# Kernel tuning notes

Hardware: AMD Instinct MI355X
Metric: run time of the kernel (lower is better)

## Reference

```python
import jax, jax.numpy as jnp
import numpy as np

N, F_IN, H, C, D, NH, L, FF = 4096, 256, 2, 64, 128, 4, 2, 2048
DEG = 32


def setup_inputs() -> dict:
    key = jax.random.key(0)
    ks = jax.random.split(key, 32)
    s = 0.05
    # graph: random edges + self loops (PyG GATConv adds self loops)
    src = jax.random.randint(ks[0], (N * DEG,), 0, N)
    dst = jax.random.randint(ks[1], (N * DEG,), 0, N)
    loop = jnp.arange(N)
    edge_index = jnp.stack([jnp.concatenate([src, loop]),
                            jnp.concatenate([dst, loop])]).astype(jnp.int64)
    inp = {
        'x': jax.random.normal(ks[2], (N, F_IN), jnp.float32),
        'edge_index': edge_index,
        'enc_w1': jax.random.normal(ks[3], (F_IN, 128), jnp.float32) * s,
        'enc_b1': jnp.zeros((128,), jnp.float32),
        'enc_w2': jax.random.normal(ks[4], (128, D), jnp.float32) * s,
        'enc_b2': jnp.zeros((D,), jnp.float32),
        'gat_w': jax.random.normal(ks[5], (D, H * C), jnp.float32) * s,
        'gat_asrc': jax.random.normal(ks[6], (H, C), jnp.float32) * s,
        'gat_adst': jax.random.normal(ks[7], (H, C), jnp.float32) * s,
        'gat_bias': jnp.zeros((H * C,), jnp.float32),
        't_wq': jax.random.normal(ks[8], (L, D, D), jnp.float32) * s,
        't_bq': jnp.zeros((L, D), jnp.float32),
        't_wk': jax.random.normal(ks[9], (L, D, D), jnp.float32) * s,
        't_bk': jnp.zeros((L, D), jnp.float32),
        't_wv': jax.random.normal(ks[10], (L, D, D), jnp.float32) * s,
        't_bv': jnp.zeros((L, D), jnp.float32),
        't_wo': jax.random.normal(ks[11], (L, D, D), jnp.float32) * s,
        't_bo': jnp.zeros((L, D), jnp.float32),
        't_ln1_g': jnp.ones((L, D), jnp.float32),
        't_ln1_b': jnp.zeros((L, D), jnp.float32),
        't_ln2_g': jnp.ones((L, D), jnp.float32),
        't_ln2_b': jnp.zeros((L, D), jnp.float32),
        't_w1': jax.random.normal(ks[12], (L, D, FF), jnp.float32) * s,
        't_b1': jnp.zeros((L, FF), jnp.float32),
        't_w2': jax.random.normal(ks[13], (L, FF, D), jnp.float32) * s,
        't_b2': jnp.zeros((L, D), jnp.float32),
    }
    return inp


def _layer_norm(v, g, b):
    m = v.mean(-1, keepdims=True)
    var = v.var(-1, keepdims=True)
    return (v - m) / jnp.sqrt(var + 1e-5) * g + b


def _forward(x, edge_index, enc_w1, enc_b1, enc_w2, enc_b2,
             gat_w, gat_asrc, gat_adst, gat_bias,
             t_wq, t_bq, t_wk, t_bk, t_wv, t_bv, t_wo, t_bo,
             t_ln1_g, t_ln1_b, t_ln2_g, t_ln2_b, t_w1, t_b1, t_w2, t_b2):
    n = x.shape[0]
    # encoder MLP: Linear -> ReLU -> Linear
    h = jnp.maximum(x @ enc_w1 + enc_b1, 0.0) @ enc_w2 + enc_b2  # [N, D]
    # GATConv (concat heads), dropout inactive (eval)
    heads, ch = gat_asrc.shape
    hh = (h @ gat_w).reshape(n, heads, ch)                       # [N, H, C]
    src, dst = edge_index[0], edge_index[1]
    a_src = (hh * gat_asrc).sum(-1)                              # [N, H]
    a_dst = (hh * gat_adst).sum(-1)
    e = jax.nn.leaky_relu(a_src[src] + a_dst[dst], 0.2)          # [E, H]
    # segment softmax over destination nodes
    e_max = jax.ops.segment_max(e, dst, num_segments=n)
    e_exp = jnp.exp(e - e_max[dst])
    denom = jax.ops.segment_sum(e_exp, dst, num_segments=n)
    alpha = e_exp / denom[dst]                                   # [E, H]
    agg = jax.ops.segment_sum(alpha[:, :, None] * hh[src], dst, num_segments=n)
    y = agg.reshape(n, heads * ch) + gat_bias                    # [N, D]
    # TransformerEncoder (post-LN, relu FFN), unbatched sequence of N nodes
    d = y.shape[-1]
    dh = d // NH
    for l in range(t_wq.shape[0]):
        q = (y @ t_wq[l] + t_bq[l]).reshape(n, NH, dh)
        k = (y @ t_wk[l] + t_bk[l]).reshape(n, NH, dh)
        v = (y @ t_wv[l] + t_bv[l]).reshape(n, NH, dh)
        scores = jnp.einsum('nhd,mhd->hnm', q, k) / jnp.sqrt(jnp.float32(dh))
        p = jax.nn.softmax(scores, axis=-1)
        a = jnp.einsum('hnm,mhd->nhd', p, v).reshape(n, d)
        a = a @ t_wo[l] + t_bo[l]
        y = _layer_norm(y + a, t_ln1_g[l], t_ln1_b[l])
        f = jnp.maximum(y @ t_w1[l] + t_b1[l], 0.0) @ t_w2[l] + t_b2[l]
        y = _layer_norm(y + f, t_ln2_g[l], t_ln2_b[l])
    return y


def reference(x, edge_index, enc_w1, enc_b1, enc_w2, enc_b2,
              gat_w, gat_asrc, gat_adst, gat_bias,
              t_wq, t_bq, t_wk, t_bk, t_wv, t_bv, t_wo, t_bo,
              t_ln1_g, t_ln1_b, t_ln2_g, t_ln2_b, t_w1, t_b1, t_w2, t_b2):
    return _forward(x, edge_index, enc_w1, enc_b1, enc_w2, enc_b2,
                    gat_w, gat_asrc, gat_adst, gat_bias,
                    t_wq, t_bq, t_wk, t_bk, t_wv, t_bv, t_wo, t_bo,
                    t_ln1_g, t_ln1_b, t_ln2_g, t_ln2_b, t_w1, t_b1, t_w2, t_b2)
```

## Files before the change

### kernel.cpp

```cpp
#include <hip/hip_runtime.h>

typedef unsigned short u16;
typedef unsigned int u32;
typedef __attribute__((ext_vector_type(8))) short bh8;
typedef __attribute__((ext_vector_type(4))) float fx4;
typedef __attribute__((ext_vector_type(4))) short s4;

#define QS 0.2550437194342803f

__device__ __forceinline__ u16 f2bf(float f) {
    unsigned u = __float_as_uint(f);
    u += 0x7fffu + ((u >> 16) & 1u);
    return (u16)(u >> 16);
}

__global__ __launch_bounds__(256) void prep_kernel(
    const float* x, const float* ew1, const float* ew2, const float* gw,
    const float* wq, const float* wk, const float* wv, const float* wo,
    const float* w1, const float* w2,
    const float* bq, const float* bk, const float* bv,
    u16* xb, u16* ew1t, u16* ew2t, u16* gwt,
    u16* wqkvt, float* bqkv, u16* wot, u16* w1t, u16* w2t)
{
    __shared__ u16 tile[64 * 65];
    int bid = blockIdx.x;
    const int t = threadIdx.x;

    if (bid < 128) {
        const float4* x4 = (const float4*)x;
        s4* o4 = (s4*)xb;
        #pragma unroll
        for (int i = 0; i < 8; i++) {
            int fi = bid * 2048 + i * 256 + t;
            float4 v = x4[fi];
            s4 o = { (short)f2bf(v.x), (short)f2bf(v.y), (short)f2bf(v.z), (short)f2bf(v.w) };
            o4[fi] = o;
        }
        return;
    }
    bid -= 128;
    if (bid < 1) {
        for (int idx = t; idx < 768; idx += 256) {
            int l = idx / 384, n = idx % 384;
            float v;
            if (n < 128)      v = bq[l * 128 + n] * QS;
            else if (n < 256) v = bk[l * 128 + n - 128];
            else              v = bv[l * 128 + n - 256];
            bqkv[idx] = v;
        }
        return;
    }
    bid -= 1;

    const float* src; u16* dst; int R, C, tr, tc; float sc = 1.f;
    if (bid < 8)            { src = ew1; dst = ew1t; R = 256; C = 128; tr = bid >> 1; tc = bid & 1; }
    else if ((bid -= 8) < 4)  { src = ew2; dst = ew2t; R = 128; C = 128; tr = bid >> 1; tc = bid & 1; }
    else if ((bid -= 4) < 4)  { src = gw;  dst = gwt;  R = 128; C = 128; tr = bid >> 1; tc = bid & 1; }
    else if ((bid -= 4) < 24) {
        int l = bid / 12, r2 = bid % 12, which = r2 >> 2, i = r2 & 3;
        R = 128; C = 128; tr = i >> 1; tc = i & 1;
        if (which == 0)      { src = wq + l * 16384; dst = wqkvt + l * 49152;         sc = QS; }
        else if (which == 1) { src = wk + l * 16384; dst = wqkvt + l * 49152 + 16384; }
        else                 { src = wv + l * 16384; dst = wqkvt + l * 49152 + 32768; }
    }
    else if ((bid -= 24) < 8)   { int l = bid >> 2, i = bid & 3;  src = wo + l * 16384; dst = wot + l * 16384; R = 128; C = 128; tr = i >> 1; tc = i & 1; }
    else if ((bid -= 8) < 128)  { int l = bid >> 6, i = bid & 63; src = w1 + (size_t)l * 262144; dst = w1t + (size_t)l * 262144; R = 128;  C = 2048; tr = i & 1;  tc = i >> 1; }
    else { bid -= 128;            int l = bid >> 6, i = bid & 63; src = w2 + (size_t)l * 262144; dst = w2t + (size_t)l * 262144; R = 2048; C = 128;  tr = i >> 1; tc = i & 1; }

    const int r = t >> 2, cs = (t & 3) * 16;
    const float* sp = src + (size_t)(tr * 64 + r) * C + tc * 64 + cs;
    #pragma unroll
    for (int j = 0; j < 16; j++) tile[r * 65 + cs + j] = f2bf(sp[j] * sc);
    __syncthreads();
    u16* dp = dst + (size_t)(tc * 64 + r) * R + tr * 64 + cs;
    #pragma unroll
    for (int j = 0; j < 16; j++) dp[j] = tile[(cs + j) * 65 + r];
}

__global__ __launch_bounds__(256) void gemm_bf16(
    const u16* __restrict__ A, const u16* __restrict__ Bt,
    const float* __restrict__ bias,
    float* __restrict__ Cf, u16* __restrict__ Cb, float* __restrict__ Cpart,
    u16* __restrict__ Cvt,
    int M, int N, int K, int relu, int kchunk, int ldc)
{
    __shared__ __align__(16) u16 As[2][64][40];
    __shared__ __align__(16) u16 Bs[2][64][40];
    const int m0 = blockIdx.x * 64, n0 = blockIdx.y * 64, z = blockIdx.z;
    const int tid = threadIdx.x;
    const int lane = tid & 63, w = tid >> 6;
    const int wm = (w >> 1) * 32, wn = (w & 1) * 32;
    const int l15 = lane & 15, l4 = lane >> 4;
    const int srow = tid >> 2, skq = (tid & 3) * 8;
    const int k0 = z * kchunk;

    const u16* Ap = A + (size_t)(m0 + srow) * K + k0 + skq;
    const u16* Bp = Bt + (size_t)(n0 + srow) * K + k0 + skq;

    fx4 acc00 = {0,0,0,0}, acc01 = {0,0,0,0}, acc10 = {0,0,0,0}, acc11 = {0,0,0,0};

    *(int4*)&As[0][srow][skq] = *(const int4*)Ap;
    *(int4*)&Bs[0][srow][skq] = *(const int4*)Bp;

    const int niter = kchunk >> 5;
    for (int it = 0; it < niter; it++) {
        const int cur = it & 1;
        int4 ar, br;
        __syncthreads();
        if (it + 1 < niter) {
            ar = *(const int4*)(Ap + (it + 1) * 32);
            br = *(const int4*)(Bp + (it + 1) * 32);
        }
        bh8 a0 = *(const bh8*)&As[cur][wm + l15][l4 * 8];
        bh8 a1 = *(const bh8*)&As[cur][wm + 16 + l15][l4 * 8];
        bh8 b0 = *(const bh8*)&Bs[cur][wn + l15][l4 * 8];
        bh8 b1 = *(const bh8*)&Bs[cur][wn + 16 + l15][l4 * 8];
        acc00 = __builtin_amdgcn_mfma_f32_16x16x32_bf16(a0, b0, acc00, 0, 0, 0);
        acc01 = __builtin_amdgcn_mfma_f32_16x16x32_bf16(a0, b1, acc01, 0, 0, 0);
        acc10 = __builtin_amdgcn_mfma_f32_16x16x32_bf16(a1, b0, acc10, 0, 0, 0);
        acc11 = __builtin_amdgcn_mfma_f32_16x16x32_bf16(a1, b1, acc11, 0, 0, 0);
        if (it + 1 < niter) {
            *(int4*)&As[cur ^ 1][srow][skq] = ar;
            *(int4*)&Bs[cur ^ 1][srow][skq] = br;
        }
    }

    fx4* accs[2][2] = {{&acc00, &acc01}, {&acc10, &acc11}};
    #pragma unroll
    for (int i = 0; i < 2; i++)
        #pragma unroll
        for (int j = 0; j < 2; j++) {
            int colg = n0 + wn + j * 16 + l15;
            int rowb = m0 + wm + i * 16 + l4 * 4;
            if (Cpart) {
                float* cp = Cpart + (size_t)z * M * N;
                #pragma unroll
                for (int r = 0; r < 4; r++)
                    cp[(size_t)(rowb + r) * N + colg] = (*accs[i][j])[r];
                continue;
            }
            float bvv = bias ? bias[colg] : 0.f;
            float vals[4];
            #pragma unroll
            for (int r = 0; r < 4; r++) {
                float v = (*accs[i][j])[r] + bvv;
                vals[r] = relu ? fmaxf(v, 0.f) : v;
            }
            if (Cvt && colg >= 256) {
                s4 pk = { (short)f2bf(vals[0]), (short)f2bf(vals[1]),
                          (short)f2bf(vals[2]), (short)f2bf(vals[3]) };
                *(s4*)&Cvt[(size_t)(colg - 256) * 4096 + rowb] = pk;
            } else {
                #pragma unroll
                for (int r = 0; r < 4; r++) {
                    if (Cf) Cf[(size_t)(rowb + r) * ldc + colg] = vals[r];
                    if (Cb) Cb[(size_t)(rowb + r) * ldc + colg] = f2bf(vals[r]);
                }
            }
        }
}

__global__ __launch_bounds__(128) void gat_prep(
    const float* __restrict__ hh, const float* __restrict__ asrc,
    const float* __restrict__ adst, float* __restrict__ an_src,
    float* __restrict__ an_dst)
{
    int n = blockIdx.x, tid = threadIdx.x;
    int head = tid >> 6, c = tid & 63;
    float v = hh[n * 128 + tid];
    float ps = v * asrc[head * 64 + c];
    float pd = v * adst[head * 64 + c];
    for (int off = 32; off; off >>= 1) { ps += __shfl_down(ps, off); pd += __shfl_down(pd, off); }
    if (c == 0) { an_src[n * 2 + head] = ps; an_dst[n * 2 + head] = pd; }
}

__global__ void count_edges(const int* __restrict__ dst, int* counts, int E) {
    int i = blockIdx.x * 256 + threadIdx.x;
    if (i < E) atomicAdd(&counts[dst[i]], 1);
}

__global__ __launch_bounds__(1024) void scan_kernel(const int* __restrict__ counts,
                                                    int* row_start, int* cursor) {
    __shared__ int s[1024];
    int tid = threadIdx.x, b = tid * 4;
    int c0 = counts[b], c1 = counts[b+1], c2 = counts[b+2], c3 = counts[b+3];
    int sum = c0 + c1 + c2 + c3;
    s[tid] = sum;
    __syncthreads();
    for (int off = 1; off < 1024; off <<= 1) {
        int v = (tid >= off) ? s[tid - off] : 0;
        __syncthreads();
        s[tid] += v;
        __syncthreads();
    }
    int excl = s[tid] - sum;
    int r0 = excl, r1 = excl + c0, r2 = r1 + c1, r3 = r2 + c2;
    row_start[b] = r0; row_start[b+1] = r1; row_start[b+2] = r2; row_start[b+3] = r3;
    cursor[b] = r0; cursor[b+1] = r1; cursor[b+2] = r2; cursor[b+3] = r3;
    if (tid == 1023) row_start[4096] = s[1023];
}

__global__ void scatter_edges(const int* __restrict__ src, const int* __restrict__ dst,
                              int* cursor, int* csr_src, int E) {
    int i = blockIdx.x * 256 + threadIdx.x;
    if (i < E) { int pos = atomicAdd(&cursor[dst[i]], 1); csr_src[pos] = src[i]; }
}

__global__ __launch_bounds__(128) void gat_aggregate(
    const int* __restrict__ row_start, const int* __restrict__ csr_src,
    const float* __restrict__ an_src, const float* __restrict__ an_dst,
    const float* __restrict__ hh, const float* __restrict__ gbias,
    float* __restrict__ y32, u16* __restrict__ yb)
{
    int n = blockIdx.x, tid = threadIdx.x;
    int start = row_start[n], end = row_start[n + 1];
    float ad0 = an_dst[n * 2 + 0], ad1 = an_dst[n * 2 + 1];

    float mx0 = -1e30f, mx1 = -1e30f;
    for (int i = start + tid; i < end; i += 128) {
        int s = csr_src[i];
        float e0 = an_src[s * 2 + 0] + ad0; e0 = e0 > 0.f ? e0 : 0.2f * e0;
        float e1 = an_src[s * 2 + 1] + ad1; e1 = e1 > 0.f ? e1 : 0.2f * e1;
        mx0 = fmaxf(mx0, e0); mx1 = fmaxf(mx1, e1);
    }
    for (int off = 32; off; off >>= 1) { mx0 = fmaxf(mx0, __shfl_down(mx0, off)); mx1 = fmaxf(mx1, __shfl_down(mx1, off)); }
    __shared__ float sm[2][2];
    if ((tid & 63) == 0) { sm[tid >> 6][0] = mx0; sm[tid >> 6][1] = mx1; }
    __syncthreads();
    mx0 = fmaxf(sm[0][0], sm[1][0]); mx1 = fmaxf(sm[0][1], sm[1][1]);

    float s0 = 0.f, s1 = 0.f;
    for (int i = start + tid; i < end; i += 128) {
        int s = csr_src[i];
        float e0 = an_src[s * 2 + 0] + ad0; e0 = e0 > 0.f ? e0 : 0.2f * e0;
        float e1 = an_src[s * 2 + 1] + ad1; e1 = e1 > 0.f ? e1 : 0.2f * e1;
        s0 += __expf(e0 - mx0); s1 += __expf(e1 - mx1);
    }
    for (int off = 32; off; off >>= 1) { s0 += __shfl_down(s0, off); s1 += __shfl_down(s1, off); }
    __shared__ float ss[2][2];
    if ((tid & 63) == 0) { ss[tid >> 6][0] = s0; ss[tid >> 6][1] = s1; }
    __syncthreads();
    s0 = ss[0][0] + ss[1][0]; s1 = ss[0][1] + ss[1][1];

    int head = tid >> 6, c = tid & 63;
    float mx = head ? mx1 : mx0, dn = head ? s1 : s0, ad = head ? ad1 : ad0;
    float agg = 0.f;
    for (int i = start; i < end; i++) {
        int s = csr_src[i];
        float e = an_src[s * 2 + head] + ad; e = e > 0.f ? e : 0.2f * e;
        agg += (__expf(e - mx) / dn) * hh[(size_t)s * 128 + head * 64 + c];
    }
    float v = agg + gbias[tid];
    y32[(size_t)n * 128 + tid] = v;
    yb[(size_t)n * 128 + tid] = f2bf(v);
}

__global__ __launch_bounds__(256) void flash_attn_part(
    const u16* __restrict__ q, const u16* __restrict__ k,
    const u16* __restrict__ vt, float* __restrict__ po,
    float* __restrict__ pm, float* __restrict__ pl)
{
    __shared__ __align__(16) u16 Kb[2][64][40];
    __shared__ __align__(16) u16 Vb[2][32][72];
    __shared__ __align__(16) u16 Ps[4][16][72];
    const int q0 = blockIdx.x * 64, h = blockIdx.y, ch = blockIdx.z;
    const int tid = threadIdx.x;
    const int w = tid >> 6, lane = tid & 63, l15 = lane & 15, l4 = lane >> 4;

    bh8 qf = *(const bh8*)&q[(size_t)(q0 + w * 16 + l15) * 256 + h * 32 + l4 * 8];

    const int skey = tid >> 2, sds = (tid & 3) * 8;
    const int svd = tid >> 3, svk = (tid & 7) * 8;
    const u16* kgp = &k[(size_t)(ch * 512 + skey) * 256 + h * 32 + sds];
    const u16* vgp = &vt[(size_t)(h * 32 + svd) * 4096 + ch * 512 + svk];

    fx4 o0 = {0,0,0,0}, o1 = {0,0,0,0};
    float M = -1e30f, L = 0.f;

    *(int4*)&Kb[0][skey][sds] = *(const int4*)kgp;
    *(int4*)&Vb[0][svd][svk] = *(const int4*)vgp;

    for (int ti = 0; ti < 8; ti++) {
        const int cur = ti & 1;
        int4 kr, vr;
        __syncthreads();
        if (ti < 7) {
            kr = *(const int4*)(kgp + (size_t)(ti + 1) * 64 * 256);
            vr = *(const int4*)(vgp + (ti + 1) * 64);
        }

        fx4 s[4];
        #pragma unroll
        for (int sub = 0; sub < 4; sub++) {
            bh8 kf = *(const bh8*)&Kb[cur][sub * 16 + l15][l4 * 8];
            fx4 z = {0,0,0,0};
            s[sub] = __builtin_amdgcn_mfma_f32_16x16x32_bf16(kf, qf, z, 0, 0, 0);
        }
        float m = fmaxf(fmaxf(s[0][0], s[0][1]), fmaxf(s[0][2], s[0][3]));
        #pragma unroll
        for (int sub = 1; sub < 4; sub++)
            m = fmaxf(m, fmaxf(fmaxf(s[sub][0], s[sub][1]), fmaxf(s[sub][2], s[sub][3])));
        m = fmaxf(m, __shfl_xor(m, 16));
        m = fmaxf(m, __shfl_xor(m, 32));
        float Mn = fmaxf(M, m);
        float f = __builtin_amdgcn_exp2f(M - Mn);
        M = Mn;
        o0 *= f; o1 *= f; L *= f;

        float lsum = 0.f;
        #pragma unroll
        for (int sub = 0; sub < 4; sub++)
            #pragma unroll
            for (int r = 0; r < 4; r++) {
                float pv = __builtin_amdgcn_exp2f(s[sub][r] - M);
                s[sub][r] = pv;
                lsum += pv;
            }
        lsum += __shfl_xor(lsum, 16);
        lsum += __shfl_xor(lsum, 32);
        L += lsum;

        #pragma unroll
        for (int sub = 0; sub < 4; sub++) {
            u32 w0 = (u32)f2bf(s[sub][0]) | ((u32)f2bf(s[sub][1]) << 16);
            u32 w1 = (u32)f2bf(s[sub][2]) | ((u32)f2bf(s[sub][3]) << 16);
            *(u32*)&Ps[w][l15][sub * 16 + l4 * 4]     = w0;
            *(u32*)&Ps[w][l15][sub * 16 + l4 * 4 + 2] = w1;
        }

        #pragma unroll
        for (int kc = 0; kc < 2; kc++) {
            bh8 bf  = *(const bh8*)&Ps[w][l15][kc * 32 + l4 * 8];
            bh8 af0 = *(const bh8*)&Vb[cur][l15][kc * 32 + l4 * 8];
            bh8 af1 = *(const bh8*)&Vb[cur][16 + l15][kc * 32 + l4 * 8];
            o0 = __builtin_amdgcn_mfma_f32_16x16x32_bf16(af0, bf, o0, 0, 0, 0);
            o1 = __builtin_amdgcn_mfma_f32_16x16x32_bf16(af1, bf, o1, 0, 0, 0);
        }

        if (ti < 7) {
            *(int4*)&Kb[cur ^ 1][skey][sds] = kr;
            *(int4*)&Vb[cur ^ 1][svd][svk] = vr;
        }
    }
    const int base = (blockIdx.x * 4 + h) * 8 + ch;
    const int qrow = w * 16 + l15;
    *(fx4*)&po[(size_t)(base * 64 + qrow) * 32 + l4 * 4]      = o0;
    *(fx4*)&po[(size_t)(base * 64 + qrow) * 32 + 16 + l4 * 4] = o1;
    if (l4 == 0) { pm[base * 64 + qrow] = M; pl[base * 64 + qrow] = L; }
}

__global__ __launch_bounds__(256) void attn_combine(
    const float* __restrict__ po, const float* __restrict__ pm,
    const float* __restrict__ pl, u16* __restrict__ out)
{
    int qb = blockIdx.x, h = blockIdx.y;
    int col = threadIdx.x & 31, r0 = threadIdx.x >> 5;
    int rb = (qb * 4 + h) * 8;
    for (int j = 0; j < 8; j++) {
        int row = r0 * 8 + j;
        float m = -1e30f;
        for (int c = 0; c < 8; c++) m = fmaxf(m, pm[(rb + c) * 64 + row]);
        float l = 0.f, o = 0.f;
        for (int c = 0; c < 8; c++) {
            float wgt = __builtin_amdgcn_exp2f(pm[(rb + c) * 64 + row] - m);
            l += wgt * pl[(rb + c) * 64 + row];
            o += wgt * po[(size_t)((rb + c) * 64 + row) * 32 + col];
        }
        out[(size_t)(qb * 64 + row) * 128 + h * 32 + col] = f2bf(o / l);
    }
}

__global__ __launch_bounds__(128) void add_ln(
    const float* __restrict__ y, const float* __restrict__ delta,
    const float* __restrict__ g, const float* __restrict__ b,
    float* __restrict__ out32, u16* __restrict__ outb)
{
    int n = blockIdx.x, tid = threadIdx.x;
    float v = y[(size_t)n * 128 + tid] + delta[(size_t)n * 128 + tid];
    float sacc = v;
    for (int off = 32; off; off >>= 1) sacc += __shfl_down(sacc, off);
    __shared__ float sm[2], sv[2];
    if ((tid & 63) == 0) sm[tid >> 6] = sacc;
    __syncthreads();
    float mean = (sm[0] + sm[1]) * (1.f / 128.f);
    float d = v - mean;
    float qacc = d * d;
    for (int off = 32; off; off >>= 1) qacc += __shfl_down(qacc, off);
    if ((tid & 63) == 0) sv[tid >> 6] = qacc;
    __syncthreads();
    float var = (sv[0] + sv[1]) * (1.f / 128.f);
    float o = d * rsqrtf(var + 1e-5f) * g[tid] + b[tid];
    out32[(size_t)n * 128 + tid] = o;
    outb[(size_t)n * 128 + tid] = f2bf(o);
}

__global__ __launch_bounds__(128) void add_ln8(
    const float* __restrict__ y, const float* __restrict__ part,
    const float* __restrict__ bias,
    const float* __restrict__ g, const float* __restrict__ b,
    float* __restrict__ out32, u16* __restrict__ outb)
{
    int n = blockIdx.x, tid = threadIdx.x;
    float v = y[(size_t)n * 128 + tid] + bias[tid];
    for (int z = 0; z < 8; z++) v += part[(size_t)z * 524288 + n * 128 + tid];
    float sacc = v;
    for (int off = 32; off; off >>= 1) sacc += __shfl_down(sacc, off);
    __shared__ float sm[2], sv[2];
    if ((tid & 63) == 0) sm[tid >> 6] = sacc;
    __syncthreads();
    float mean = (sm[0] + sm[1]) * (1.f / 128.f);
    float d = v - mean;
    float qacc = d * d;
    for (int off = 32; off; off >>= 1) qacc += __shfl_down(qacc, off);
    if ((tid & 63) == 0) sv[tid >> 6] = qacc;
    __syncthreads();
    float var = (sv[0] + sv[1]) * (1.f / 128.f);
    float o = d * rsqrtf(var + 1e-5f) * g[tid] + b[tid];
    out32[(size_t)n * 128 + tid] = o;
    outb[(size_t)n * 128 + tid] = f2bf(o);
}

extern "C" void kernel_launch(void* const* d_in, const int* in_sizes, int n_in,
                              void* d_out, int out_size, void* d_ws, size_t ws_size,
                              hipStream_t stream)
{
    const float* x     = (const float*)d_in[0];
    const int*   ei    = (const int*)  d_in[1];
    const float* ew1   = (const float*)d_in[2];
    const float* eb1   = (const float*)d_in[3];
    const float* ew2   = (const float*)d_in[4];
    const float* eb2   = (const float*)d_in[5];
    const float* gw    = (const float*)d_in[6];
    const float* gasrc = (const float*)d_in[7];
    const float* gadst = (const float*)d_in[8];
    const float* gbias = (const float*)d_in[9];
    const float* wq    = (const float*)d_in[10];
    const float* bq    = (const float*)d_in[11];
    const float* wk    = (const float*)d_in[12];
    const float* bk    = (const float*)d_in[13];
    const float* wv    = (const float*)d_in[14];
    const float* bv    = (const float*)d_in[15];
    const float* wo    = (const float*)d_in[16];
    const float* bo    = (const float*)d_in[17];
    const float* ln1g  = (const float*)d_in[18];
    const float* ln1b  = (const float*)d_in[19];
    const float* ln2g  = (const float*)d_in[20];
    const float* ln2b  = (const float*)d_in[21];
    const float* w1    = (const float*)d_in[22];
    const float* b1    = (const float*)d_in[23];
    const float* w2    = (const float*)d_in[24];
    const float* b2    = (const float*)d_in[25];

    const int E = in_sizes[1] / 2;
    const int* esrc = ei;
    const int* edst = ei + E;

    char* p = (char*)d_ws;
    auto alloc = [&](size_t bytes) -> void* {
        void* r = (void*)p;
        p += (bytes + 255) & ~(size_t)255;
        return r;
    };
    u16* xb    = (u16*)alloc(4096 * 256 * 2);
    u16* ew1t  = (u16*)alloc(128 * 256 * 2);
    u16* ew2t  = (u16*)alloc(128 * 128 * 2);
    u16* gwt   = (u16*)alloc(128 * 128 * 2);
    u16* wqkvt = (u16*)alloc(2 * 384 * 128 * 2);
    float* bqkv = (float*)alloc(2 * 384 * 4);
    u16* wot   = (u16*)alloc(2 * 128 * 128 * 2);
    u16* w1t   = (u16*)alloc(2 * 2048 * 128 * 2);
    u16* w2t   = (u16*)alloc(2 * 128 * 2048 * 2);
    u16* h1b   = (u16*)alloc(4096 * 128 * 2);
    u16* hb    = (u16*)alloc(4096 * 128 * 2);
    float* hh  = (float*)alloc(4096 * 128 * 4);
    float* ansrc = (float*)alloc(4096 * 2 * 4);
    float* andst = (float*)alloc(4096 * 2 * 4);
    int* counts    = (int*)alloc(4096 * 4);
    int* row_start = (int*)alloc(4097 * 4);
    int* cursor    = (int*)alloc(4096 * 4);
    int* csr_src   = (int*)alloc((size_t)E * 4);
    float* y32 = (float*)alloc(4096 * 128 * 4);
    u16* yb    = (u16*)alloc(4096 * 128 * 2);
    u16* qkvb  = (u16*)alloc((size_t)4096 * 256 * 2);
    u16* vtb   = (u16*)alloc(4096 * 128 * 2);
    u16* attnb = (u16*)alloc(4096 * 128 * 2);
    float* po  = (float*)alloc((size_t)64 * 4 * 8 * 64 * 32 * 4);
    float* pm  = (float*)alloc(64 * 4 * 8 * 64 * 4);
    float* pl  = (float*)alloc(64 * 4 * 8 * 64 * 4);
    float* proj32 = (float*)alloc(4096 * 128 * 4);
    u16* ff1b  = (u16*)alloc((size_t)4096 * 2048 * 2);
    float* ff2part = (float*)alloc((size_t)8 * 4096 * 128 * 4);

    prep_kernel<<<433, 256, 0, stream>>>(x, ew1, ew2, gw, wq, wk, wv, wo, w1, w2,
                                         bq, bk, bv,
                                         xb, ew1t, ew2t, gwt, wqkvt, bqkv, wot, w1t, w2t);

    gemm_bf16<<<dim3(64, 2), 256, 0, stream>>>(xb, ew1t, eb1, nullptr, h1b, nullptr, nullptr, 4096, 128, 256, 1, 256, 128);
    gemm_bf16<<<dim3(64, 2), 256, 0, stream>>>(h1b, ew2t, eb2, nullptr, hb, nullptr, nullptr, 4096, 128, 128, 0, 128, 128);

    gemm_bf16<<<dim3(64, 2), 256, 0, stream>>>(hb, gwt, nullptr, hh, nullptr, nullptr, nullptr, 4096, 128, 128, 0, 128, 128);
    gat_prep<<<4096, 128, 0, stream>>>(hh, gasrc, gadst, ansrc, andst);
    hipMemsetAsync(counts, 0, 4096 * sizeof(int), stream);
    count_edges<<<(E + 255) / 256, 256, 0, stream>>>(edst, counts, E);
    scan_kernel<<<1, 1024, 0, stream>>>(counts, row_start, cursor);
    scatter_edges<<<(E + 255) / 256, 256, 0, stream>>>(esrc, edst, cursor, csr_src, E);
    gat_aggregate<<<4096, 128, 0, stream>>>(row_start, csr_src, ansrc, andst, hh, gbias, y32, yb);

    for (int l = 0; l < 2; l++) {
        gemm_bf16<<<dim3(64, 6), 256, 0, stream>>>(yb, wqkvt + l * 49152, bqkv + l * 384, nullptr, qkvb, nullptr, vtb, 4096, 384, 128, 0, 128, 256);
        flash_attn_part<<<dim3(64, 4, 8), 256, 0, stream>>>(qkvb, qkvb + 128, vtb, po, pm, pl);
        attn_combine<<<dim3(64, 4), 256, 0, stream>>>(po, pm, pl, attnb);
        gemm_bf16<<<dim3(64, 2), 256, 0, stream>>>(attnb, wot + l * 16384, bo + l * 128, proj32, nullptr, nullptr, nullptr, 4096, 128, 128, 0, 128, 128);
        add_ln<<<4096, 128, 0, stream>>>(y32, proj32, ln1g + l * 128, ln1b + l * 128, y32, yb);
        gemm_bf16<<<dim3(64, 32), 256, 0, stream>>>(yb, w1t + (size_t)l * 262144, b1 + l * 2048, nullptr, ff1b, nullptr, nullptr, 4096, 2048, 128, 1, 128, 2048);
        gemm_bf16<<<dim3(64, 2, 8), 256, 0, stream>>>(ff1b, w2t + (size_t)l * 262144, nullptr, nullptr, nullptr, ff2part, nullptr, 4096, 128, 2048, 0, 256, 128);
        float* outp = (l == 1) ? (float*)d_out : y32;
        add_ln8<<<4096, 128, 0, stream>>>(y32, ff2part, b2 + l * 128, ln2g + l * 128, ln2b + l * 128, outp, yb);
    }
}
```

Baseline: 216.3 us.

## Template GEMM tile sizes per call and widen GAT aggregation blocks

Turns the fixed 64x64 bf16 MFMA GEMM into a template over block tile sizes. Each call now gets its own tile: 128x128 for the FFN GEMMs for more register reuse, and 32x64 for the small 128-wide GEMMs to launch more blocks. The GAT aggregation goes from 128 to 256 threads, splitting the edge loop across two groups and adding a shared-memory reduction at the end. Flash-attention LDS padding also changes from 72 to 68. Larger tiles raise register pressure and cut the block count for the FFN GEMMs, and the 68 padding may alter LDS bank conflicts.

```diff
diff --git a/kernel.cpp b/kernel.cpp
--- a/kernel.cpp
+++ b/kernel.cpp
@@ -77,73 +77,80 @@
     for (int j = 0; j < 16; j++) dp[j] = tile[(cs + j) * 65 + r];
 }
 
-__global__ __launch_bounds__(256) void gemm_bf16(
+template<int BM, int BN>
+__global__ __launch_bounds__(256) void gemm_t(
     const u16* __restrict__ A, const u16* __restrict__ Bt,
     const float* __restrict__ bias,
     float* __restrict__ Cf, u16* __restrict__ Cb, float* __restrict__ Cpart,
     u16* __restrict__ Cvt,
     int M, int N, int K, int relu, int kchunk, int ldc)
 {
-    __shared__ __align__(16) u16 As[2][64][40];
-    __shared__ __align__(16) u16 Bs[2][64][40];
-    const int m0 = blockIdx.x * 64, n0 = blockIdx.y * 64, z = blockIdx.z;
+    constexpr int NM = BM / 32, NN = BN / 32;
+    constexpr int ASL = BM * 4, BSL = BN * 4;
+    constexpr int ANI = (ASL + 255) / 256, BNI = (BSL + 255) / 256;
+    __shared__ __align__(16) u16 As[2][BM][40];
+    __shared__ __align__(16) u16 Bs[2][BN][40];
+    const int m0 = blockIdx.x * BM, n0 = blockIdx.y * BN, z = blockIdx.z;
     const int tid = threadIdx.x;
     const int lane = tid & 63, w = tid >> 6;
-    const int wm = (w >> 1) * 32, wn = (w & 1) * 32;
+    const int wm = (w >> 1) * (BM / 2), wn = (w & 1) * (BN / 2);
     const int l15 = lane & 15, l4 = lane >> 4;
-    const int srow = tid >> 2, skq = (tid & 3) * 8;
     const int k0 = z * kchunk;
 
-    const u16* Ap = A + (size_t)(m0 + srow) * K + k0 + skq;
-    const u16* Bp = Bt + (size_t)(n0 + srow) * K + k0 + skq;
-
-    fx4 acc00 = {0,0,0,0}, acc01 = {0,0,0,0}, acc10 = {0,0,0,0}, acc11 = {0,0,0,0};
-
-    *(int4*)&As[0][srow][skq] = *(const int4*)Ap;
-    *(int4*)&Bs[0][srow][skq] = *(const int4*)Bp;
+    fx4 acc[NM][NN] = {};
+
+    #pragma unroll
+    for (int i = 0; i < ANI; i++) { int s = tid + i * 256; if (s < ASL) { int r = s >> 2, c = (s & 3) * 8; *(int4*)&As[0][r][c] = *(const int4*)&A[(size_t)(m0 + r) * K + k0 + c]; } }
+    #pragma unroll
+    for (int i = 0; i < BNI; i++) { int s = tid + i * 256; if (s < BSL) { int r = s >> 2, c = (s & 3) * 8; *(int4*)&Bs[0][r][c] = *(const int4*)&Bt[(size_t)(n0 + r) * K + k0 + c]; } }
 
     const int niter = kchunk >> 5;
     for (int it = 0; it < niter; it++) {
         const int cur = it & 1;
-        int4 ar, br;
+        int4 ar[ANI], br[BNI];
         __syncthreads();
         if (it + 1 < niter) {
-            ar = *(const int4*)(Ap + (it + 1) * 32);
-            br = *(const int4*)(Bp + (it + 1) * 32);
-        }
-        bh8 a0 = *(const bh8*)&As[cur][wm + l15][l4 * 8];
-        bh8 a1 = *(const bh8*)&As[cur][wm + 16 + l15][l4 * 8];
-        bh8 b0 = *(const bh8*)&Bs[cur][wn + l15][l4 * 8];
-        bh8 b1 = *(const bh8*)&Bs[cur][wn + 16 + l15][l4 * 8];
-        acc00 = __builtin_amdgcn_mfma_f32_16x16x32_bf16(a0, b0, acc00, 0, 0, 0);
-        acc01 = __builtin_amdgcn_mfma_f32_16x16x32_bf16(a0, b1, acc01, 0, 0, 0);
-        acc10 = __builtin_amdgcn_mfma_f32_16x16x32_bf16(a1, b0, acc10, 0, 0, 0);
-        acc11 = __builtin_amdgcn_mfma_f32_16x16x32_bf16(a1, b1, acc11, 0, 0, 0);
+            #pragma unroll
+            for (int i = 0; i < ANI; i++) { int s = tid + i * 256; if (s < ASL) { int r = s >> 2, c = (s & 3) * 8; ar[i] = *(const int4*)&A[(size_t)(m0 + r) * K + k0 + (it + 1) * 32 + c]; } }
+            #pragma unroll
+            for (int i = 0; i < BNI; i++) { int s = tid + i * 256; if (s < BSL) { int r = s >> 2, c = (s & 3) * 8; br[i] = *(const int4*)&Bt[(size_t)(n0 + r) * K + k0 + (it + 1) * 32 + c]; } }
+        }
+        bh8 af[NM], bf[NN];
+        #pragma unroll
+        for (int mi = 0; mi < NM; mi++) af[mi] = *(const bh8*)&As[cur][wm + mi * 16 + l15][l4 * 8];
+        #pragma unroll
+        for (int nj = 0; nj < NN; nj++) bf[nj] = *(const bh8*)&Bs[cur][wn + nj * 16 + l15][l4 * 8];
+        #pragma unroll
+        for (int mi = 0; mi < NM; mi++)
+            #pragma unroll
+            for (int nj = 0; nj < NN; nj++)
+                acc[mi][nj] = __builtin_amdgcn_mfma_f32_16x16x32_bf16(af[mi], bf[nj], acc[mi][nj], 0, 0, 0);
         if (it + 1 < niter) {
-            *(int4*)&As[cur ^ 1][srow][skq] = ar;
-            *(int4*)&Bs[cur ^ 1][srow][skq] = br;
-        }
-    }
-
-    fx4* accs[2][2] = {{&acc00, &acc01}, {&acc10, &acc11}};
+            #pragma unroll
+            for (int i = 0; i < ANI; i++) { int s = tid + i * 256; if (s < ASL) { int r = s >> 2, c = (s & 3) * 8; *(int4*)&As[cur ^ 1][r][c] = ar[i]; } }
+            #pragma unroll
+            for (int i = 0; i < BNI; i++) { int s = tid + i * 256; if (s < BSL) { int r = s >> 2, c = (s & 3) * 8; *(int4*)&Bs[cur ^ 1][r][c] = br[i]; } }
+        }
+    }
+
     #pragma unroll
-    for (int i = 0; i < 2; i++)
-        #pragma unroll
-        for (int j = 0; j < 2; j++) {
-            int colg = n0 + wn + j * 16 + l15;
-            int rowb = m0 + wm + i * 16 + l4 * 4;
+    for (int mi = 0; mi < NM; mi++)
+        #pragma unroll
+        for (int nj = 0; nj < NN; nj++) {
+            int colg = n0 + wn + nj * 16 + l15;
+            int rowb = m0 + wm + mi * 16 + l4 * 4;
             if (Cpart) {
                 float* cp = Cpart + (size_t)z * M * N;
                 #pragma unroll
                 for (int r = 0; r < 4; r++)
-                    cp[(size_t)(rowb + r) * N + colg] = (*accs[i][j])[r];
+                    cp[(size_t)(rowb + r) * N + colg] = acc[mi][nj][r];
                 continue;
             }
             float bvv = bias ? bias[colg] : 0.f;
             float vals[4];
             #pragma unroll
             for (int r = 0; r < 4; r++) {
-                float v = (*accs[i][j])[r] + bvv;
+                float v = acc[mi][nj][r] + bvv;
                 vals[r] = relu ? fmaxf(v, 0.f) : v;
             }
             if (Cvt && colg >= 256) {
@@ -206,53 +213,59 @@
     if (i < E) { int pos = atomicAdd(&cursor[dst[i]], 1); csr_src[pos] = src[i]; }
 }
 
-__global__ __launch_bounds__(128) void gat_aggregate(
+__global__ __launch_bounds__(256) void gat_aggregate(
     const int* __restrict__ row_start, const int* __restrict__ csr_src,
     const float* __restrict__ an_src, const float* __restrict__ an_dst,
     const float* __restrict__ hh, const float* __restrict__ gbias,
     float* __restrict__ y32, u16* __restrict__ yb)
 {
     int n = blockIdx.x, tid = threadIdx.x;
+    const int lane = tid & 63, wv = tid >> 6;
     int start = row_start[n], end = row_start[n + 1];
     float ad0 = an_dst[n * 2 + 0], ad1 = an_dst[n * 2 + 1];
+    __shared__ float rmx[4][2], rsm[4][2], sagg[256];
 
     float mx0 = -1e30f, mx1 = -1e30f;
-    for (int i = start + tid; i < end; i += 128) {
+    for (int i = start + tid; i < end; i += 256) {
         int s = csr_src[i];
         float e0 = an_src[s * 2 + 0] + ad0; e0 = e0 > 0.f ? e0 : 0.2f * e0;
         float e1 = an_src[s * 2 + 1] + ad1; e1 = e1 > 0.f ? e1 : 0.2f * e1;
         mx0 = fmaxf(mx0, e0); mx1 = fmaxf(mx1, e1);
     }
     for (int off = 32; off; off >>= 1) { mx0 = fmaxf(mx0, __shfl_down(mx0, off)); mx1 = fmaxf(mx1, __shfl_down(mx1, off)); }
-    __shared__ float sm[2][2];
-    if ((tid & 63) == 0) { sm[tid >> 6][0] = mx0; sm[tid >> 6][1] = mx1; }
-    __syncthreads();
-    mx0 = fmaxf(sm[0][0], sm[1][0]); mx1 = fmaxf(sm[0][1], sm[1][1]);
+    if (lane == 0) { rmx[wv][0] = mx0; rmx[wv][1] = mx1; }
+    __syncthreads();
+    mx0 = fmaxf(fmaxf(rmx[0][0], rmx[1][0]), fmaxf(rmx[2][0], rmx[3][0]));
+    mx1 = fmaxf(fmaxf(rmx[0][1], rmx[1][1]), fmaxf(rmx[2][1], rmx[3][1]));
 
     float s0 = 0.f, s1 = 0.f;
-    for (int i = start + tid; i < end; i += 128) {
+    for (int i = start + tid; i < end; i += 256) {
         int s = csr_src[i];
         float e0 = an_src[s * 2 + 0] + ad0; e0 = e0 > 0.f ? e0 : 0.2f * e0;
         float e1 = an_src[s * 2 + 1] + ad1; e1 = e1 > 0.f ? e1 : 0.2f * e1;
         s0 += __expf(e0 - mx0); s1 += __expf(e1 - mx1);
     }
     for (int off = 32; off; off >>= 1) { s0 += __shfl_down(s0, off); s1 += __shfl_down(s1, off); }
-    __shared__ float ss[2][2];
-    if ((tid & 63) == 0) { ss[tid >> 6][0] = s0; ss[tid >> 6][1] = s1; }
-    __syncthreads();
-    s0 = ss[0][0] + ss[1][0]; s1 = ss[0][1] + ss[1][1];
-
-    int head = tid >> 6, c = tid & 63;
+    if (lane == 0) { rsm[wv][0] = s0; rsm[wv][1] = s1; }
+    __syncthreads();
+    s0 = rsm[0][0] + rsm[1][0] + rsm[2][0] + rsm[3][0];
+    s1 = rsm[0][1] + rsm[1][1] + rsm[2][1] + rsm[3][1];
+
+    const int grp = tid >> 7, ch = tid & 127, head = ch >> 6;
     float mx = head ? mx1 : mx0, dn = head ? s1 : s0, ad = head ? ad1 : ad0;
     float agg = 0.f;
-    for (int i = start; i < end; i++) {
+    for (int i = start + grp; i < end; i += 2) {
         int s = csr_src[i];
         float e = an_src[s * 2 + head] + ad; e = e > 0.f ? e : 0.2f * e;
-        agg += (__expf(e - mx) / dn) * hh[(size_t)s * 128 + head * 64 + c];
-    }
-    float v = agg + gbias[tid];
-    y32[(size_t)n * 128 + tid] = v;
-    yb[(size_t)n * 128 + tid] = f2bf(v);
+        agg += (__expf(e - mx) / dn) * hh[(size_t)s * 128 + ch];
+    }
+    sagg[tid] = agg;
+    __syncthreads();
+    if (tid < 128) {
+        float v = sagg[tid] + sagg[tid + 128] + gbias[tid];
+        y32[(size_t)n * 128 + tid] = v;
+        yb[(size_t)n * 128 + tid] = f2bf(v);
+    }
 }
 
 __global__ __launch_bounds__(256) void flash_attn_part(
@@ -261,8 +274,8 @@
     float* __restrict__ pm, float* __restrict__ pl)
 {
     __shared__ __align__(16) u16 Kb[2][64][40];
-    __shared__ __align__(16) u16 Vb[2][32][72];
-    __shared__ __align__(16) u16 Ps[4][16][72];
+    __shared__ __align__(16) u16 Vb[2][32][68];
+    __shared__ __align__(16) u16 Ps[4][16][68];
     const int q0 = blockIdx.x * 64, h = blockIdx.y, ch = blockIdx.z;
     const int tid = threadIdx.x;
     const int w = tid >> 6, lane = tid & 63, l15 = lane & 15, l4 = lane >> 4;
@@ -495,25 +508,25 @@
                                          bq, bk, bv,
                                          xb, ew1t, ew2t, gwt, wqkvt, bqkv, wot, w1t, w2t);
 
-    gemm_bf16<<<dim3(64, 2), 256, 0, stream>>>(xb, ew1t, eb1, nullptr, h1b, nullptr, nullptr, 4096, 128, 256, 1, 256, 128);
-    gemm_bf16<<<dim3(64, 2), 256, 0, stream>>>(h1b, ew2t, eb2, nullptr, hb, nullptr, nullptr, 4096, 128, 128, 0, 128, 128);
-
-    gemm_bf16<<<dim3(64, 2), 256, 0, stream>>>(hb, gwt, nullptr, hh, nullptr, nullptr, nullptr, 4096, 128, 128, 0, 128, 128);
+    gemm_t<32, 64><<<dim3(128, 2), 256, 0, stream>>>(xb, ew1t, eb1, nullptr, h1b, nullptr, nullptr, 4096, 128, 256, 1, 256, 128);
+    gemm_t<32, 64><<<dim3(128, 2), 256, 0, stream>>>(h1b, ew2t, eb2, nullptr, hb, nullptr, nullptr, 4096, 128, 128, 0, 128, 128);
+
+    gemm_t<32, 64><<<dim3(128, 2), 256, 0, stream>>>(hb, gwt, nullptr, hh, nullptr, nullptr, nullptr, 4096, 128, 128, 0, 128, 128);
     gat_prep<<<4096, 128, 0, stream>>>(hh, gasrc, gadst, ansrc, andst);
     hipMemsetAsync(counts, 0, 4096 * sizeof(int), stream);
     count_edges<<<(E + 255) / 256, 256, 0, stream>>>(edst, counts, E);
     scan_kernel<<<1, 1024, 0, stream>>>(counts, row_start, cursor);
     scatter_edges<<<(E + 255) / 256, 256, 0, stream>>>(esrc, edst, cursor, csr_src, E);
-    gat_aggregate<<<4096, 128, 0, stream>>>(row_start, csr_src, ansrc, andst, hh, gbias, y32, yb);
+    gat_aggregate<<<4096, 256, 0, stream>>>(row_start, csr_src, ansrc, andst, hh, gbias, y32, yb);
 
     for (int l = 0; l < 2; l++) {
-        gemm_bf16<<<dim3(64, 6), 256, 0, stream>>>(yb, wqkvt + l * 49152, bqkv + l * 384, nullptr, qkvb, nullptr, vtb, 4096, 384, 128, 0, 128, 256);
+        gemm_t<64, 64><<<dim3(64, 6), 256, 0, stream>>>(yb, wqkvt + l * 49152, bqkv + l * 384, nullptr, qkvb, nullptr, vtb, 4096, 384, 128, 0, 128, 256);
         flash_attn_part<<<dim3(64, 4, 8), 256, 0, stream>>>(qkvb, qkvb + 128, vtb, po, pm, pl);
         attn_combine<<<dim3(64, 4), 256, 0, stream>>>(po, pm, pl, attnb);
-        gemm_bf16<<<dim3(64, 2), 256, 0, stream>>>(attnb, wot + l * 16384, bo + l * 128, proj32, nullptr, nullptr, nullptr, 4096, 128, 128, 0, 128, 128);
+        gemm_t<32, 64><<<dim3(128, 2), 256, 0, stream>>>(attnb, wot + l * 16384, bo + l * 128, proj32, nullptr, nullptr, nullptr, 4096, 128, 128, 0, 128, 128);
         add_ln<<<4096, 128, 0, stream>>>(y32, proj32, ln1g + l * 128, ln1b + l * 128, y32, yb);
-        gemm_bf16<<<dim3(64, 32), 256, 0, stream>>>(yb, w1t + (size_t)l * 262144, b1 + l * 2048, nullptr, ff1b, nullptr, nullptr, 4096, 2048, 128, 1, 128, 2048);
-        gemm_bf16<<<dim3(64, 2, 8), 256, 0, stream>>>(ff1b, w2t + (size_t)l * 262144, nullptr, nullptr, nullptr, ff2part, nullptr, 4096, 128, 2048, 0, 256, 128);
+        gemm_t<128, 128><<<dim3(32, 16), 256, 0, stream>>>(yb, w1t + (size_t)l * 262144, b1 + l * 2048, nullptr, ff1b, nullptr, nullptr, 4096, 2048, 128, 1, 128, 2048);
+        gemm_t<128, 128><<<dim3(32, 1, 8), 256, 0, stream>>>(ff1b, w2t + (size_t)l * 262144, nullptr, nullptr, nullptr, ff2part, nullptr, 4096, 128, 2048, 0, 256, 128);
         float* outp = (l == 1) ? (float*)d_out : y32;
         add_ln8<<<4096, 128, 0, stream>>>(y32, ff2part, b2 + l * 128, ln2g + l * 128, ln2b + l * 128, outp, yb);
     }
```

Result: slower. 260.0 us (+20.2%).

## Parallelize GAT aggregation with shared attention weights; lazy rescale in flash attention

Applied to the files above, without the earlier changes.

The GAT aggregation kernel now uses 256 threads. It stages per-edge normalized attention coefficients and source indices in shared memory in chunks of 128, and two thread groups split the edges before a final shared-memory reduction. This removes the redundant per-channel recomputation of exp and the division on the serial edge loop. The flash attention kernel skips rescaling the running output unless the new maximum exceeds the old one by more than 8 (log2 domain). It also uses tree-shaped max/sum reductions and the hardware v_cvt_pk_bf16_f32 instruction to pack probabilities. The lazy rescale can let exponentials grow up to 2^8 before renormalizing, which carries a small precision risk.

```diff
diff --git a/kernel.cpp b/kernel.cpp
--- a/kernel.cpp
+++ b/kernel.cpp
@@ -5,6 +5,7 @@
 typedef __attribute__((ext_vector_type(8))) short bh8;
 typedef __attribute__((ext_vector_type(4))) float fx4;
 typedef __attribute__((ext_vector_type(4))) short s4;
+typedef __attribute__((ext_vector_type(2))) unsigned int u32x2;
 
 #define QS 0.2550437194342803f
 
@@ -12,6 +13,12 @@
     unsigned u = __float_as_uint(f);
     u += 0x7fffu + ((u >> 16) & 1u);
     return (u16)(u >> 16);
+}
+
+__device__ __forceinline__ u32 cvtpk(float lo, float hi) {
+    u32 r;
+    asm("v_cvt_pk_bf16_f32 %0, %1, %2" : "=v"(r) : "v"(lo), "v"(hi));
+    return r;
 }
 
 __global__ __launch_bounds__(256) void prep_kernel(
@@ -206,53 +213,72 @@
     if (i < E) { int pos = atomicAdd(&cursor[dst[i]], 1); csr_src[pos] = src[i]; }
 }
 
-__global__ __launch_bounds__(128) void gat_aggregate(
+__global__ __launch_bounds__(256) void gat_aggregate(
     const int* __restrict__ row_start, const int* __restrict__ csr_src,
     const float* __restrict__ an_src, const float* __restrict__ an_dst,
     const float* __restrict__ hh, const float* __restrict__ gbias,
     float* __restrict__ y32, u16* __restrict__ yb)
 {
     int n = blockIdx.x, tid = threadIdx.x;
+    const int lane = tid & 63, wv = tid >> 6;
     int start = row_start[n], end = row_start[n + 1];
     float ad0 = an_dst[n * 2 + 0], ad1 = an_dst[n * 2 + 1];
+    __shared__ float rmx[4][2], rsm[4][2];
+    __shared__ float sal0[128], sal1[128], sagg[256];
+    __shared__ int sidx[128];
 
     float mx0 = -1e30f, mx1 = -1e30f;
-    for (int i = start + tid; i < end; i += 128) {
+    for (int i = start + tid; i < end; i += 256) {
         int s = csr_src[i];
         float e0 = an_src[s * 2 + 0] + ad0; e0 = e0 > 0.f ? e0 : 0.2f * e0;
         float e1 = an_src[s * 2 + 1] + ad1; e1 = e1 > 0.f ? e1 : 0.2f * e1;
         mx0 = fmaxf(mx0, e0); mx1 = fmaxf(mx1, e1);
     }
     for (int off = 32; off; off >>= 1) { mx0 = fmaxf(mx0, __shfl_down(mx0, off)); mx1 = fmaxf(mx1, __shfl_down(mx1, off)); }
-    __shared__ float sm[2][2];
-    if ((tid & 63) == 0) { sm[tid >> 6][0] = mx0; sm[tid >> 6][1] = mx1; }
-    __syncthreads();
-    mx0 = fmaxf(sm[0][0], sm[1][0]); mx1 = fmaxf(sm[0][1], sm[1][1]);
-
-    float s0 = 0.f, s1 = 0.f;
-    for (int i = start + tid; i < end; i += 128) {
+    if (lane == 0) { rmx[wv][0] = mx0; rmx[wv][1] = mx1; }
+    __syncthreads();
+    mx0 = fmaxf(fmaxf(rmx[0][0], rmx[1][0]), fmaxf(rmx[2][0], rmx[3][0]));
+    mx1 = fmaxf(fmaxf(rmx[0][1], rmx[1][1]), fmaxf(rmx[2][1], rmx[3][1]));
+
+    float den0 = 0.f, den1 = 0.f;
+    for (int i = start + tid; i < end; i += 256) {
         int s = csr_src[i];
         float e0 = an_src[s * 2 + 0] + ad0; e0 = e0 > 0.f ? e0 : 0.2f * e0;
         float e1 = an_src[s * 2 + 1] + ad1; e1 = e1 > 0.f ? e1 : 0.2f * e1;
-        s0 += __expf(e0 - mx0); s1 += __expf(e1 - mx1);
-    }
-    for (int off = 32; off; off >>= 1) { s0 += __shfl_down(s0, off); s1 += __shfl_down(s1, off); }
-    __shared__ float ss[2][2];
-    if ((tid & 63) == 0) { ss[tid >> 6][0] = s0; ss[tid >> 6][1] = s1; }
-    __syncthreads();
-    s0 = ss[0][0] + ss[1][0]; s1 = ss[0][1] + ss[1][1];
-
-    int head = tid >> 6, c = tid & 63;
-    float mx = head ? mx1 : mx0, dn = head ? s1 : s0, ad = head ? ad1 : ad0;
+        den0 += __expf(e0 - mx0); den1 += __expf(e1 - mx1);
+    }
+    for (int off = 32; off; off >>= 1) { den0 += __shfl_down(den0, off); den1 += __shfl_down(den1, off); }
+    if (lane == 0) { rsm[wv][0] = den0; rsm[wv][1] = den1; }
+    __syncthreads();
+    den0 = rsm[0][0] + rsm[1][0] + rsm[2][0] + rsm[3][0];
+    den1 = rsm[0][1] + rsm[1][1] + rsm[2][1] + rsm[3][1];
+    float rd0 = 1.f / den0, rd1 = 1.f / den1;
+
+    const int grp = tid >> 7, ch = tid & 127, head = ch >> 6;
     float agg = 0.f;
-    for (int i = start; i < end; i++) {
-        int s = csr_src[i];
-        float e = an_src[s * 2 + head] + ad; e = e > 0.f ? e : 0.2f * e;
-        agg += (__expf(e - mx) / dn) * hh[(size_t)s * 128 + head * 64 + c];
-    }
-    float v = agg + gbias[tid];
-    y32[(size_t)n * 128 + tid] = v;
-    yb[(size_t)n * 128 + tid] = f2bf(v);
+    for (int c0 = start; c0 < end; c0 += 128) {
+        int cnt = min(128, end - c0);
+        __syncthreads();
+        if (tid < cnt) {
+            int s = csr_src[c0 + tid];
+            float e0 = an_src[s * 2 + 0] + ad0; e0 = e0 > 0.f ? e0 : 0.2f * e0;
+            float e1 = an_src[s * 2 + 1] + ad1; e1 = e1 > 0.f ? e1 : 0.2f * e1;
+            sal0[tid] = __expf(e0 - mx0) * rd0;
+            sal1[tid] = __expf(e1 - mx1) * rd1;
+            sidx[tid] = s;
+        }
+        __syncthreads();
+        const float* sal = head ? sal1 : sal0;
+        for (int j = grp; j < cnt; j += 2)
+            agg += sal[j] * hh[(size_t)sidx[j] * 128 + ch];
+    }
+    sagg[tid] = agg;
+    __syncthreads();
+    if (tid < 128) {
+        float v = sagg[tid] + sagg[tid + 128] + gbias[tid];
+        y32[(size_t)n * 128 + tid] = v;
+        yb[(size_t)n * 128 + tid] = f2bf(v);
+    }
 }
 
 __global__ __launch_bounds__(256) void flash_attn_part(
@@ -296,36 +322,38 @@
             fx4 z = {0,0,0,0};
             s[sub] = __builtin_amdgcn_mfma_f32_16x16x32_bf16(kf, qf, z, 0, 0, 0);
         }
-        float m = fmaxf(fmaxf(s[0][0], s[0][1]), fmaxf(s[0][2], s[0][3]));
-        #pragma unroll
-        for (int sub = 1; sub < 4; sub++)
-            m = fmaxf(m, fmaxf(fmaxf(s[sub][0], s[sub][1]), fmaxf(s[sub][2], s[sub][3])));
-        m = fmaxf(m, __shfl_xor(m, 16));
-        m = fmaxf(m, __shfl_xor(m, 32));
-        float Mn = fmaxf(M, m);
-        float f = __builtin_amdgcn_exp2f(M - Mn);
-        M = Mn;
-        o0 *= f; o1 *= f; L *= f;
-
-        float lsum = 0.f;
+        float t0 = fmaxf(fmaxf(s[0][0], s[0][1]), s[0][2]);
+        float t1 = fmaxf(fmaxf(s[0][3], s[1][0]), s[1][1]);
+        float t2 = fmaxf(fmaxf(s[1][2], s[1][3]), s[2][0]);
+        float t3 = fmaxf(fmaxf(s[2][1], s[2][2]), s[2][3]);
+        float t4 = fmaxf(fmaxf(s[3][0], s[3][1]), s[3][2]);
+        float pmax = fmaxf(fmaxf(fmaxf(t0, t1), t2), fmaxf(fmaxf(t3, t4), s[3][3]));
+        pmax = fmaxf(pmax, __shfl_xor(pmax, 16));
+        pmax = fmaxf(pmax, __shfl_xor(pmax, 32));
+        if (!__all(pmax - M <= 8.0f)) {
+            float f = __builtin_amdgcn_exp2f(M - pmax);
+            M = pmax;
+            o0 *= f; o1 *= f; L *= f;
+        }
+
         #pragma unroll
         for (int sub = 0; sub < 4; sub++)
             #pragma unroll
-            for (int r = 0; r < 4; r++) {
-                float pv = __builtin_amdgcn_exp2f(s[sub][r] - M);
-                s[sub][r] = pv;
-                lsum += pv;
-            }
+            for (int r = 0; r < 4; r++)
+                s[sub][r] = __builtin_amdgcn_exp2f(s[sub][r] - M);
+        float ss0 = (s[0][0] + s[0][1]) + (s[0][2] + s[0][3]);
+        float ss1 = (s[1][0] + s[1][1]) + (s[1][2] + s[1][3]);
+        float ss2 = (s[2][0] + s[2][1]) + (s[2][2] + s[2][3]);
+        float ss3 = (s[3][0] + s[3][1]) + (s[3][2] + s[3][3]);
+        float lsum = (ss0 + ss1) + (ss2 + ss3);
         lsum += __shfl_xor(lsum, 16);
         lsum += __shfl_xor(lsum, 32);
         L += lsum;
 
         #pragma unroll
         for (int sub = 0; sub < 4; sub++) {
-            u32 w0 = (u32)f2bf(s[sub][0]) | ((u32)f2bf(s[sub][1]) << 16);
-            u32 w1 = (u32)f2bf(s[sub][2]) | ((u32)f2bf(s[sub][3]) << 16);
-            *(u32*)&Ps[w][l15][sub * 16 + l4 * 4]     = w0;
-            *(u32*)&Ps[w][l15][sub * 16 + l4 * 4 + 2] = w1;
+            u32x2 pk = { cvtpk(s[sub][0], s[sub][1]), cvtpk(s[sub][2], s[sub][3]) };
+            *(u32x2*)&Ps[w][l15][sub * 16 + l4 * 4] = pk;
         }
 
         #pragma unroll
@@ -504,7 +532,7 @@
     count_edges<<<(E + 255) / 256, 256, 0, stream>>>(edst, counts, E);
     scan_kernel<<<1, 1024, 0, stream>>>(counts, row_start, cursor);
     scatter_edges<<<(E + 255) / 256, 256, 0, stream>>>(esrc, edst, cursor, csr_src, E);
-    gat_aggregate<<<4096, 128, 0, stream>>>(row_start, csr_src, ansrc, andst, hh, gbias, y32, yb);
+    gat_aggregate<<<4096, 256, 0, stream>>>(row_start, csr_src, ansrc, andst, hh, gbias, y32, yb);
 
     for (int l = 0; l < 2; l++) {
         gemm_bf16<<<dim3(64, 6), 256, 0, stream>>>(yb, wqkvt + l * 49152, bqkv + l * 384, nullptr, qkvb, nullptr, vtb, 4096, 384, 128, 0, 128, 256);
```

New measurement: 209.8 us. 3.0% less time.
